# Kernel tuning notes

Measured on AMD Instinct MI355X. Metric: run time of the kernel, lower is better.

Reference implementation:

```python
import jax, jax.numpy as jnp
import numpy as np

N = 200000
E = 6400000
IN_F = 128
HID = 128
OUT_F = 16
LAYERS = 3
EPS = 1e-5


def setup_inputs() -> dict:
    key = jax.random.key(0)
    ks = jax.random.split(key, 12)
    nodes = jax.random.normal(ks[0], (N, IN_F), dtype=jnp.float32)
    src = jax.random.randint(ks[1], (E,), 0, N, dtype=jnp.int32)
    dst = jax.random.randint(ks[2], (E,), 0, N, dtype=jnp.int32)
    s_in = 1.0 / np.sqrt(IN_F)
    s_h = 1.0 / np.sqrt(HID)
    W_in = jax.random.uniform(ks[3], (IN_F, HID), jnp.float32, -s_in, s_in)
    b_in = jax.random.uniform(ks[4], (HID,), jnp.float32, -s_in, s_in)
    Ws = jax.random.uniform(ks[5], (LAYERS, HID, HID), jnp.float32, -s_h, s_h)
    bs = jax.random.uniform(ks[6], (LAYERS, HID), jnp.float32, -s_h, s_h)
    gammas = jnp.ones((LAYERS, HID), jnp.float32)
    betas = jnp.zeros((LAYERS, HID), jnp.float32)
    W_out = jax.random.uniform(ks[7], (HID, OUT_F), jnp.float32, -s_h, s_h)
    b_out = jax.random.uniform(ks[8], (OUT_F,), jnp.float32, -s_h, s_h)
    return {"nodes": nodes, "src": src, "dst": dst, "W_in": W_in, "b_in": b_in,
            "Ws": Ws, "bs": bs, "gammas": gammas, "betas": betas,
            "W_out": W_out, "b_out": b_out}


def _layernorm(x, g, b):
    mu = jnp.mean(x, axis=-1, keepdims=True)
    var = jnp.var(x, axis=-1, keepdims=True)
    return (x - mu) * jax.lax.rsqrt(var + EPS) * g + b


def reference(nodes, src, dst, W_in, b_in, Ws, bs, gammas, betas, W_out, b_out):
    # in-degree for 'gcn' aggregator normalization: (sum_neigh + self) / (deg + 1)
    deg = jax.ops.segment_sum(jnp.ones((E,), jnp.float32), dst, num_segments=N)
    inv = 1.0 / (deg + 1.0)  # [N]
    x = nodes @ W_in + b_in  # [N, HID]
    for l in range(LAYERS):
        agg = jax.ops.segment_sum(x[src], dst, num_segments=N)  # gather+scatter-add
        h = (agg + x) * inv[:, None]          # gcn mean incl. self
        h = h @ Ws[l] + bs[l]                 # fc_neigh
        h = jax.nn.relu(h)                    # activation (before norm, per DGL)
        x = _layernorm(h, gammas[l], betas[l])
    return x @ W_out + b_out  # [N, OUT_F]
```

## Files before the change

kernel.cpp:

```cpp
#include <hip/hip_runtime.h>

#define N_NODES 200000
#define N_EDGES 6400000
#define HID 128
#define OUTF 16
#define LAYERS 3
#define EPS 1e-5f

#define NRANGES 16
#define RANGE_N 12500
#define NBUCKETS 800
#define BUCKET_N 250
#define BATCH 5000
#define NBATCH (N_EDGES / BATCH)
#define RCAP 405000
#define RBLK (RCAP / BATCH)
#define BCAP 9500

#define FTILE 32

typedef unsigned int u32;

__device__ __forceinline__ unsigned short f2bf(float f){
  unsigned int u = __float_as_uint(f);
  u += 0x7fffu + ((u >> 16) & 1u);
  return (unsigned short)(u >> 16);
}
__device__ __forceinline__ u32 pack2bf(float lo, float hi){
  return (u32)f2bf(lo) | ((u32)f2bf(hi) << 16);
}


__global__ __launch_bounds__(256) void k_initcur(int* __restrict__ range_cursor,
                                                 int* __restrict__ bucket_cursor){
  int t = blockIdx.x * 256 + threadIdx.x;
  if (t < NRANGES) range_cursor[t] = t * RCAP;
  if (t < NBUCKETS) bucket_cursor[t] = t * BCAP;
}


__global__ __launch_bounds__(256) void k_p1(const int* __restrict__ src, const int* __restrict__ dst,
                                            int* __restrict__ range_cursor, u32* __restrict__ ebuf1){
  __shared__ u32 stage[BATCH];
  __shared__ int hist[NRANGES], hist2[NRANGES], hbase[NRANGES], gbase[NRANGES];
  const int tid = threadIdx.x;
  const long e0 = (long)blockIdx.x * BATCH;

  if (tid < NRANGES){ hist[tid] = 0; hist2[tid] = 0; }
  __syncthreads();
  for (int i = tid; i < BATCH; i += 256){
    int d = dst[e0 + i];
    atomicAdd(&hist[d / RANGE_N], 1);
  }
  __syncthreads();
  if (tid == 0){ int run = 0; for (int b = 0; b < NRANGES; b++){ hbase[b] = run; run += hist[b]; } }
  __syncthreads();
  if (tid < NRANGES && hist[tid] > 0) gbase[tid] = atomicAdd(&range_cursor[tid], hist[tid]);
  __syncthreads();
  for (int i = tid; i < BATCH; i += 256){
    int d = dst[e0 + i];
    int s = src[e0 + i];
    int r = d / RANGE_N;
    u32 pk = ((u32)(d - r * RANGE_N) << 18) | (u32)s;
    int p = atomicAdd(&hist2[r], 1);
    stage[hbase[r] + p] = pk;
  }
  __syncthreads();
  for (int b = 0; b < NRANGES; b++){
    int len = hist[b];
    int gb = gbase[b], hb = hbase[b];
    for (int i = tid; i < len; i += 256) ebuf1[gb + i] = stage[hb + i];
  }
}


__global__ __launch_bounds__(256) void k_p2(const u32* __restrict__ ebuf1, const int* __restrict__ range_cursor,
                                            int* __restrict__ bucket_cursor, u32* __restrict__ ebuf2){
  __shared__ u32 stage[BATCH];
  __shared__ int hist[50], hist2[50], hbase[50], gbase[50];
  const int tid = threadIdx.x;
  const int r = blockIdx.x / RBLK;
  const int chunk = blockIdx.x % RBLK;
  const int rlen = range_cursor[r] - r * RCAP;
  const int i0 = chunk * BATCH;
  const int len = min(BATCH, rlen - i0);
  if (len <= 0) return;
  const u32* seg = ebuf1 + (long)r * RCAP + i0;

  if (tid < 50){ hist[tid] = 0; hist2[tid] = 0; }
  __syncthreads();
  for (int i = tid; i < len; i += 256){
    int dl = (int)(seg[i] >> 18);
    atomicAdd(&hist[dl / BUCKET_N], 1);
  }
  __syncthreads();
  if (tid == 0){ int run = 0; for (int b = 0; b < 50; b++){ hbase[b] = run; run += hist[b]; } }
  __syncthreads();
  if (tid < 50 && hist[tid] > 0) gbase[tid] = atomicAdd(&bucket_cursor[r * 50 + tid], hist[tid]);
  __syncthreads();
  for (int i = tid; i < len; i += 256){
    u32 pk = seg[i];
    int b = (int)(pk >> 18) / BUCKET_N;
    int p = atomicAdd(&hist2[b], 1);
    stage[hbase[b] + p] = pk;
  }
  __syncthreads();
  for (int b = 0; b < 50; b++){
    int l = hist[b];
    if (l == 0) continue;
    int gb = gbase[b], hb = hbase[b];
    for (int i = tid; i < l; i += 256) ebuf2[gb + i] = stage[hb + i];
  }
}


__global__ __launch_bounds__(256) void k_scanb(const int* __restrict__ bucket_cursor,
                                               int* __restrict__ bucket_base){
  __shared__ int q[256];
  int tid = threadIdx.x;
  int v[4]; int sum4 = 0;
  if (tid < 200){
    #pragma unroll
    for (int j = 0; j < 4; j++){ int b = 4 * tid + j; v[j] = bucket_cursor[b] - b * BCAP; sum4 += v[j]; }
  }
  q[tid] = sum4; __syncthreads();
  for (int off = 1; off < 256; off <<= 1){
    int t = (tid >= off) ? q[tid - off] : 0;
    __syncthreads();
    q[tid] += t;
    __syncthreads();
  }
  if (tid < 200){
    int run = q[tid] - sum4;
    #pragma unroll
    for (int j = 0; j < 4; j++){ bucket_base[4 * tid + j] = run; run += v[j]; }
  }
}


__global__ __launch_bounds__(256) void k_p3(const u32* __restrict__ ebuf2, const int* __restrict__ bucket_cursor,
                                            const int* __restrict__ bucket_base,
                                            int* __restrict__ csr, int* __restrict__ row_start){
  __shared__ int stage[BCAP];
  __shared__ int hist[BUCKET_N], sbase[BUCKET_N], cur[BUCKET_N];
  __shared__ int q[256];
  const int tid = threadIdx.x;
  const int b = blockIdx.x;
  const int n0 = b * BUCKET_N;
  const int dl0 = (b % 50) * BUCKET_N;
  const int len = min(bucket_cursor[b] - b * BCAP, BCAP);
  const int base = bucket_base[b];
  const u32* seg = ebuf2 + (long)b * BCAP;

  if (tid < BUCKET_N){ hist[tid] = 0; cur[tid] = 0; }
  __syncthreads();
  for (int i = tid; i < len; i += 256){
    int local = (int)(seg[i] >> 18) - dl0;
    local = min(max(local, 0), BUCKET_N - 1);
    atomicAdd(&hist[local], 1);
  }
  __syncthreads();
  {
    int v = (tid < BUCKET_N) ? hist[tid] : 0;
    q[tid] = v; __syncthreads();
    for (int off = 1; off < 256; off <<= 1){
      int t = (tid >= off) ? q[tid - off] : 0;
      __syncthreads();
      q[tid] += t;
      __syncthreads();
    }
    if (tid < BUCKET_N) sbase[tid] = q[tid] - v;
  }
  __syncthreads();
  for (int i = tid; i < len; i += 256){
    u32 pk = seg[i];
    int local = (int)(pk >> 18) - dl0;
    local = min(max(local, 0), BUCKET_N - 1);
    int pos = atomicAdd(&cur[local], 1);
    stage[sbase[local] + pos] = (int)(pk & 0x3FFFFu);
  }
  __syncthreads();
  for (int i = tid; i < len; i += 256) csr[base + i] = stage[i];
  if (tid < BUCKET_N) row_start[n0 + tid] = base + sbase[tid];
  if (b == NBUCKETS - 1 && tid == 0) row_start[N_NODES] = base + len;
}


__global__ __launch_bounds__(256) void k_gemm128(const float* __restrict__ A,
    const float* __restrict__ W, const float* __restrict__ bias,
    u32* __restrict__ xbout)
{
  __shared__ float As[64][132];
  const int tid = threadIdx.x;
  const long row0 = (long)blockIdx.x * 64;

  const float4* A4 = (const float4*)(A + row0 * HID);
  for (int i = tid; i < 64 * 32; i += 256){
    int r = i >> 5, c = i & 31;
    *(float4*)&As[r][c * 4] = A4[r * 32 + c];
  }
  __syncthreads();

  const int cg = tid & 31;
  const int rg = tid >> 5;
  const int c0 = cg * 4;
  float acc[8][4];
  {
    float4 b = *(const float4*)&bias[c0];
    #pragma unroll
    for (int r = 0; r < 8; r++){ acc[r][0]=b.x; acc[r][1]=b.y; acc[r][2]=b.z; acc[r][3]=b.w; }
  }

  for (int k = 0; k < HID; k += 4){
    float4 w0 = *(const float4*)&W[(k + 0) * HID + c0];
    float4 w1 = *(const float4*)&W[(k + 1) * HID + c0];
    float4 w2 = *(const float4*)&W[(k + 2) * HID + c0];
    float4 w3 = *(const float4*)&W[(k + 3) * HID + c0];
    #pragma unroll
    for (int r = 0; r < 8; r++){
      float4 a = *(const float4*)&As[rg * 8 + r][k];
      acc[r][0] = fmaf(a.w, w3.x, fmaf(a.z, w2.x, fmaf(a.y, w1.x, fmaf(a.x, w0.x, acc[r][0]))));
      acc[r][1] = fmaf(a.w, w3.y, fmaf(a.z, w2.y, fmaf(a.y, w1.y, fmaf(a.x, w0.y, acc[r][1]))));
      acc[r][2] = fmaf(a.w, w3.z, fmaf(a.z, w2.z, fmaf(a.y, w1.z, fmaf(a.x, w0.z, acc[r][2]))));
      acc[r][3] = fmaf(a.w, w3.w, fmaf(a.z, w2.w, fmaf(a.y, w1.w, fmaf(a.x, w0.w, acc[r][3]))));
    }
  }

  #pragma unroll
  for (int r = 0; r < 8; r++){
    long row = row0 + rg * 8 + r;
    uint2 p; p.x = pack2bf(acc[r][0], acc[r][1]); p.y = pack2bf(acc[r][2], acc[r][3]);
    *(uint2*)&xbout[(row * HID + c0) >> 1] = p;
  }
}


__global__ __launch_bounds__(256) void k_fused(const int* __restrict__ row_start,
    const int* __restrict__ csr, const uint2* __restrict__ xb2,
    const float* __restrict__ W, const float* __restrict__ bias,
    const float* __restrict__ gamma, const float* __restrict__ beta,
    u32* __restrict__ xbout)
{
  __shared__ float As[FTILE][132];
  const int tid = threadIdx.x;
  const long row0 = (long)blockIdx.x * FTILE;

  {
    const int wv = tid >> 6;
    const int lane = tid & 63;
    const int half = lane >> 5, col = lane & 31;
    const uint2* xbc = xb2 + col;

    for (int i = 0; i < FTILE / 4; i++){
      const int r = wv * (FTILE / 4) + i;
      const int node = (int)row0 + r;
      const int s0 = row_start[node], s1 = row_start[node + 1];

      float4 xs = {0.f, 0.f, 0.f, 0.f};
      if (half == 0){
        uint2 sv = xb2[(long)node * 32 + col];
        xs.x = __uint_as_float(sv.x << 16);
        xs.y = __uint_as_float(sv.x & 0xffff0000u);
        xs.z = __uint_as_float(sv.y << 16);
        xs.w = __uint_as_float(sv.y & 0xffff0000u);
      }

      float a0 = 0.f, a1 = 0.f, a2 = 0.f, a3 = 0.f;
      int base = s0;
      int idx[8];
      if (base + 16 <= s1){
        #pragma unroll
        for (int j = 0; j < 8; j++) idx[j] = csr[base + 2*j + half];
      }
      while (base + 16 <= s1){
        uint2 p[8];
        #pragma unroll
        for (int j = 0; j < 8; j++) p[j] = xbc[(long)idx[j] * 32];
        base += 16;
        if (base + 16 <= s1){
          #pragma unroll
          for (int j = 0; j < 8; j++) idx[j] = csr[base + 2*j + half];
        }
        #pragma unroll
        for (int j = 0; j < 8; j++){
          a0 += __uint_as_float(p[j].x << 16);
          a1 += __uint_as_float(p[j].x & 0xffff0000u);
          a2 += __uint_as_float(p[j].y << 16);
          a3 += __uint_as_float(p[j].y & 0xffff0000u);
        }
      }
      if (base < s1){
        const int s1m1 = s1 - 1;
        int ti[8];
        #pragma unroll
        for (int j = 0; j < 8; j++) ti[j] = csr[min(base + 2*j + half, s1m1)];
        uint2 p[8];
        #pragma unroll
        for (int j = 0; j < 8; j++) p[j] = xbc[(long)ti[j] * 32];
        #pragma unroll
        for (int j = 0; j < 8; j++){
          bool act = (base + 2*j + half) < s1;
          float v0 = __uint_as_float(p[j].x << 16);
          float v1 = __uint_as_float(p[j].x & 0xffff0000u);
          float v2 = __uint_as_float(p[j].y << 16);
          float v3 = __uint_as_float(p[j].y & 0xffff0000u);
          a0 += act ? v0 : 0.f;
          a1 += act ? v1 : 0.f;
          a2 += act ? v2 : 0.f;
          a3 += act ? v3 : 0.f;
        }
      }

      a0 += __shfl_down(a0, 32);
      a1 += __shfl_down(a1, 32);
      a2 += __shfl_down(a2, 32);
      a3 += __shfl_down(a3, 32);

      if (half == 0){
        float inv = 1.f / (float)(s1 - s0 + 1);
        float4 rv;
        rv.x = (a0 + xs.x) * inv;
        rv.y = (a1 + xs.y) * inv;
        rv.z = (a2 + xs.z) * inv;
        rv.w = (a3 + xs.w) * inv;
        *(float4*)&As[r][col * 4] = rv;
      }
    }
  }
  __syncthreads();

  const int cg = tid & 31;
  const int rg = tid >> 5;
  const int c0 = cg * 4;
  float acc[4][4];
  {
    float4 b = *(const float4*)&bias[c0];
    #pragma unroll
    for (int r = 0; r < 4; r++){ acc[r][0]=b.x; acc[r][1]=b.y; acc[r][2]=b.z; acc[r][3]=b.w; }
  }

  for (int k = 0; k < HID; k += 4){
    float4 w0 = *(const float4*)&W[(k + 0) * HID + c0];
    float4 w1 = *(const float4*)&W[(k + 1) * HID + c0];
    float4 w2 = *(const float4*)&W[(k + 2) * HID + c0];
    float4 w3 = *(const float4*)&W[(k + 3) * HID + c0];
    #pragma unroll
    for (int r = 0; r < 4; r++){
      float4 a = *(const float4*)&As[rg * 4 + r][k];
      acc[r][0] = fmaf(a.w, w3.x, fmaf(a.z, w2.x, fmaf(a.y, w1.x, fmaf(a.x, w0.x, acc[r][0]))));
      acc[r][1] = fmaf(a.w, w3.y, fmaf(a.z, w2.y, fmaf(a.y, w1.y, fmaf(a.x, w0.y, acc[r][1]))));
      acc[r][2] = fmaf(a.w, w3.z, fmaf(a.z, w2.z, fmaf(a.y, w1.z, fmaf(a.x, w0.z, acc[r][2]))));
      acc[r][3] = fmaf(a.w, w3.w, fmaf(a.z, w2.w, fmaf(a.y, w1.w, fmaf(a.x, w0.w, acc[r][3]))));
    }
  }

  float s[4], s2[4];
  #pragma unroll
  for (int r = 0; r < 4; r++){
    float v0 = fmaxf(acc[r][0], 0.f);
    float v1 = fmaxf(acc[r][1], 0.f);
    float v2 = fmaxf(acc[r][2], 0.f);
    float v3 = fmaxf(acc[r][3], 0.f);
    acc[r][0] = v0; acc[r][1] = v1; acc[r][2] = v2; acc[r][3] = v3;
    s[r]  = (v0 + v1) + (v2 + v3);
    s2[r] = fmaf(v0, v0, fmaf(v1, v1, fmaf(v2, v2, v3 * v3)));
  }
  #pragma unroll
  for (int m = 1; m < 32; m <<= 1){
    #pragma unroll
    for (int r = 0; r < 4; r++){
      s[r]  += __shfl_xor(s[r],  m);
      s2[r] += __shfl_xor(s2[r], m);
    }
  }

  const float4 gm = *(const float4*)&gamma[c0];
  const float4 bt = *(const float4*)&beta[c0];
  #pragma unroll
  for (int r = 0; r < 4; r++){
    float mu = s[r] * (1.f / HID);
    float var = s2[r] * (1.f / HID) - mu * mu;
    float rs = 1.f / sqrtf(var + EPS);
    float4 v;
    v.x = (acc[r][0] - mu) * rs * gm.x + bt.x;
    v.y = (acc[r][1] - mu) * rs * gm.y + bt.y;
    v.z = (acc[r][2] - mu) * rs * gm.z + bt.z;
    v.w = (acc[r][3] - mu) * rs * gm.w + bt.w;
    long row = row0 + rg * 4 + r;
    uint2 p; p.x = pack2bf(v.x, v.y); p.y = pack2bf(v.z, v.w);
    *(uint2*)&xbout[(row * HID + c0) >> 1] = p;
  }
}


__global__ __launch_bounds__(256) void k_gemm_out(const u32* __restrict__ xb,
    const float* __restrict__ Wo, const float* __restrict__ bo, float* __restrict__ out)
{
  __shared__ float As[16][132];
  __shared__ float Wl[HID * OUTF];
  const int tid = threadIdx.x;
  const long row0 = (long)blockIdx.x * 16;
  {
    int r = tid >> 4, u = tid & 15;
    uint4 v = ((const uint4*)xb)[(row0 + r) * 16 + u];
    float* d = &As[r][u * 8];
    d[0] = __uint_as_float(v.x << 16); d[1] = __uint_as_float(v.x & 0xffff0000u);
    d[2] = __uint_as_float(v.y << 16); d[3] = __uint_as_float(v.y & 0xffff0000u);
    d[4] = __uint_as_float(v.z << 16); d[5] = __uint_as_float(v.z & 0xffff0000u);
    d[6] = __uint_as_float(v.w << 16); d[7] = __uint_as_float(v.w & 0xffff0000u);
  }
  for (int i = tid; i < HID * OUTF; i += 256) Wl[i] = Wo[i];
  __syncthreads();
  int col = tid & 15, r = tid >> 4;
  float acc = bo[col];
  for (int k = 0; k < HID; k += 4){
    float4 a = *(const float4*)&As[r][k];
    acc = fmaf(a.x, Wl[(k + 0) * OUTF + col],
          fmaf(a.y, Wl[(k + 1) * OUTF + col],
          fmaf(a.z, Wl[(k + 2) * OUTF + col],
          fmaf(a.w, Wl[(k + 3) * OUTF + col], acc))));
  }
  out[(row0 + r) * OUTF + col] = acc;
}


extern "C" void kernel_launch(void* const* d_in, const int* in_sizes, int n_in,
                              void* d_out, int out_size, void* d_ws, size_t ws_size,
                              hipStream_t stream)
{
  (void)in_sizes; (void)n_in; (void)out_size; (void)ws_size;
  const float* nodes = (const float*)d_in[0];
  const int*   src   = (const int*)d_in[1];
  const int*   dst   = (const int*)d_in[2];
  const float* W_in  = (const float*)d_in[3];
  const float* b_in  = (const float*)d_in[4];
  const float* Ws    = (const float*)d_in[5];
  const float* bs    = (const float*)d_in[6];
  const float* gam   = (const float*)d_in[7];
  const float* bet   = (const float*)d_in[8];
  const float* W_out = (const float*)d_in[9];
  const float* b_out = (const float*)d_in[10];
  float* out = (float*)d_out;

  size_t off = 0;
  auto bump = [&](size_t bytes) -> char* {
    char* p = (char*)d_ws + off;
    off = (off + bytes + 255) & ~(size_t)255;
    return p;
  };
  int* row_start     = (int*)bump((N_NODES + 1) * sizeof(int));
  int* range_cursor  = (int*)bump(NRANGES * sizeof(int));
  int* bucket_cursor = (int*)bump(NBUCKETS * sizeof(int));
  int* bucket_base   = (int*)bump((NBUCKETS + 1) * sizeof(int));
  int* csr           = (int*)bump((size_t)N_EDGES * sizeof(int));
  u32* xb0           = (u32*)bump((size_t)N_NODES * HID * sizeof(unsigned short));
  u32* xb1           = (u32*)bump((size_t)N_NODES * HID * sizeof(unsigned short));

  u32* ebuf1 = (u32*)xb0;
  u32* ebuf2 = (u32*)xb1;

  k_initcur<<<4, 256, 0, stream>>>(range_cursor, bucket_cursor);
  k_p1<<<NBATCH, 256, 0, stream>>>(src, dst, range_cursor, ebuf1);
  k_p2<<<NRANGES * RBLK, 256, 0, stream>>>(ebuf1, range_cursor, bucket_cursor, ebuf2);
  k_scanb<<<1, 256, 0, stream>>>(bucket_cursor, bucket_base);
  k_p3<<<NBUCKETS, 256, 0, stream>>>(ebuf2, bucket_cursor, bucket_base, csr, row_start);

  k_gemm128<<<N_NODES / 64, 256, 0, stream>>>(nodes, W_in, b_in, xb0);

  const u32* xbi = xb0; u32* xbo = xb1;
  for (int l = 0; l < LAYERS; l++){
    k_fused<<<N_NODES / FTILE, 256, 0, stream>>>(row_start, csr, (const uint2*)xbi,
                                                 Ws + (size_t)l * HID * HID, bs + l * HID,
                                                 gam + l * HID, bet + l * HID, xbo);
    const u32* tb = xbi; xbi = xbo; xbo = (u32*)tb;
  }

  k_gemm_out<<<N_NODES / 16, 256, 0, stream>>>(xbi, W_out, b_out, out);
}
```

Before: 1.218 ms.

## Merge input GEMM into edge partition kernel and fuse output projection into last layer

The first edge-partition pass and the input projection GEMM now run in one launch, with block ranges split between the two tasks. ebuf1 gets its own workspace buffer so the GEMM output does not collide with it. The last layer's aggregate+GEMM+LayerNorm kernel now also applies the output projection in-block, so the final bf16 activations are never written out and read back. The cost is extra workspace memory and a larger last-layer kernel that may hold more registers.

```diff
diff --git a/kernel.cpp b/kernel.cpp
--- a/kernel.cpp
+++ b/kernel.cpp
@@ -39,37 +39,90 @@
 }
 
 
-__global__ __launch_bounds__(256) void k_p1(const int* __restrict__ src, const int* __restrict__ dst,
-                                            int* __restrict__ range_cursor, u32* __restrict__ ebuf1){
-  __shared__ u32 stage[BATCH];
-  __shared__ int hist[NRANGES], hist2[NRANGES], hbase[NRANGES], gbase[NRANGES];
+__global__ __launch_bounds__(256) void k_front(const int* __restrict__ src, const int* __restrict__ dst,
+    int* __restrict__ range_cursor, u32* __restrict__ ebuf1,
+    const float* __restrict__ A, const float* __restrict__ W,
+    const float* __restrict__ bias, u32* __restrict__ xbout)
+{
+  __shared__ __align__(16) char smraw[64 * 132 * 4];
   const int tid = threadIdx.x;
-  const long e0 = (long)blockIdx.x * BATCH;
-
-  if (tid < NRANGES){ hist[tid] = 0; hist2[tid] = 0; }
-  __syncthreads();
-  for (int i = tid; i < BATCH; i += 256){
-    int d = dst[e0 + i];
-    atomicAdd(&hist[d / RANGE_N], 1);
-  }
-  __syncthreads();
-  if (tid == 0){ int run = 0; for (int b = 0; b < NRANGES; b++){ hbase[b] = run; run += hist[b]; } }
-  __syncthreads();
-  if (tid < NRANGES && hist[tid] > 0) gbase[tid] = atomicAdd(&range_cursor[tid], hist[tid]);
-  __syncthreads();
-  for (int i = tid; i < BATCH; i += 256){
-    int d = dst[e0 + i];
-    int s = src[e0 + i];
-    int r = d / RANGE_N;
-    u32 pk = ((u32)(d - r * RANGE_N) << 18) | (u32)s;
-    int p = atomicAdd(&hist2[r], 1);
-    stage[hbase[r] + p] = pk;
-  }
-  __syncthreads();
-  for (int b = 0; b < NRANGES; b++){
-    int len = hist[b];
-    int gb = gbase[b], hb = hbase[b];
-    for (int i = tid; i < len; i += 256) ebuf1[gb + i] = stage[hb + i];
+
+  if (blockIdx.x < NBATCH){
+    u32* stage = (u32*)smraw;
+    int* hist  = (int*)(smraw + 20000);
+    int* hist2 = hist + 16;
+    int* hbase = hist + 32;
+    int* gbase = hist + 48;
+    const long e0 = (long)blockIdx.x * BATCH;
+
+    if (tid < NRANGES){ hist[tid] = 0; hist2[tid] = 0; }
+    __syncthreads();
+    for (int i = tid; i < BATCH; i += 256){
+      int d = dst[e0 + i];
+      atomicAdd(&hist[d / RANGE_N], 1);
+    }
+    __syncthreads();
+    if (tid == 0){ int run = 0; for (int b = 0; b < NRANGES; b++){ hbase[b] = run; run += hist[b]; } }
+    __syncthreads();
+    if (tid < NRANGES && hist[tid] > 0) gbase[tid] = atomicAdd(&range_cursor[tid], hist[tid]);
+    __syncthreads();
+    for (int i = tid; i < BATCH; i += 256){
+      int d = dst[e0 + i];
+      int s = src[e0 + i];
+      int r = d / RANGE_N;
+      u32 pk = ((u32)(d - r * RANGE_N) << 18) | (u32)s;
+      int p = atomicAdd(&hist2[r], 1);
+      stage[hbase[r] + p] = pk;
+    }
+    __syncthreads();
+    for (int b = 0; b < NRANGES; b++){
+      int len = hist[b];
+      int gb = gbase[b], hb = hbase[b];
+      for (int i = tid; i < len; i += 256) ebuf1[gb + i] = stage[hb + i];
+    }
+    return;
+  }
+
+  float (*As)[132] = (float (*)[132])smraw;
+  const long row0 = (long)(blockIdx.x - NBATCH) * 64;
+
+  const float4* A4 = (const float4*)(A + row0 * HID);
+  for (int i = tid; i < 64 * 32; i += 256){
+    int r = i >> 5, c = i & 31;
+    *(float4*)&As[r][c * 4] = A4[r * 32 + c];
+  }
+  __syncthreads();
+
+  const int cg = tid & 31;
+  const int rg = tid >> 5;
+  const int c0 = cg * 4;
+  float acc[8][4];
+  {
+    float4 b = *(const float4*)&bias[c0];
+    #pragma unroll
+    for (int r = 0; r < 8; r++){ acc[r][0]=b.x; acc[r][1]=b.y; acc[r][2]=b.z; acc[r][3]=b.w; }
+  }
+
+  for (int k = 0; k < HID; k += 4){
+    float4 w0 = *(const float4*)&W[(k + 0) * HID + c0];
+    float4 w1 = *(const float4*)&W[(k + 1) * HID + c0];
+    float4 w2 = *(const float4*)&W[(k + 2) * HID + c0];
+    float4 w3 = *(const float4*)&W[(k + 3) * HID + c0];
+    #pragma unroll
+    for (int r = 0; r < 8; r++){
+      float4 a = *(const float4*)&As[rg * 8 + r][k];
+      acc[r][0] = fmaf(a.w, w3.x, fmaf(a.z, w2.x, fmaf(a.y, w1.x, fmaf(a.x, w0.x, acc[r][0]))));
+      acc[r][1] = fmaf(a.w, w3.y, fmaf(a.z, w2.y, fmaf(a.y, w1.y, fmaf(a.x, w0.y, acc[r][1]))));
+      acc[r][2] = fmaf(a.w, w3.z, fmaf(a.z, w2.z, fmaf(a.y, w1.z, fmaf(a.x, w0.z, acc[r][2]))));
+      acc[r][3] = fmaf(a.w, w3.w, fmaf(a.z, w2.w, fmaf(a.y, w1.w, fmaf(a.x, w0.w, acc[r][3]))));
+    }
+  }
+
+  #pragma unroll
+  for (int r = 0; r < 8; r++){
+    long row = row0 + rg * 8 + r;
+    uint2 p; p.x = pack2bf(acc[r][0], acc[r][1]); p.y = pack2bf(acc[r][2], acc[r][3]);
+    *(uint2*)&xbout[(row * HID + c0) >> 1] = p;
   }
 }
 
@@ -186,51 +239,89 @@
 }
 
 
-__global__ __launch_bounds__(256) void k_gemm128(const float* __restrict__ A,
-    const float* __restrict__ W, const float* __restrict__ bias,
-    u32* __restrict__ xbout)
+__device__ __forceinline__ void agg_tile(const int* __restrict__ row_start,
+    const int* __restrict__ csr, const uint2* __restrict__ xb2,
+    long row0, int tid, float (*As)[132])
 {
-  __shared__ float As[64][132];
-  const int tid = threadIdx.x;
-  const long row0 = (long)blockIdx.x * 64;
-
-  const float4* A4 = (const float4*)(A + row0 * HID);
-  for (int i = tid; i < 64 * 32; i += 256){
-    int r = i >> 5, c = i & 31;
-    *(float4*)&As[r][c * 4] = A4[r * 32 + c];
-  }
-  __syncthreads();
-
-  const int cg = tid & 31;
-  const int rg = tid >> 5;
-  const int c0 = cg * 4;
-  float acc[8][4];
-  {
-    float4 b = *(const float4*)&bias[c0];
-    #pragma unroll
-    for (int r = 0; r < 8; r++){ acc[r][0]=b.x; acc[r][1]=b.y; acc[r][2]=b.z; acc[r][3]=b.w; }
-  }
-
-  for (int k = 0; k < HID; k += 4){
-    float4 w0 = *(const float4*)&W[(k + 0) * HID + c0];
-    float4 w1 = *(const float4*)&W[(k + 1) * HID + c0];
-    float4 w2 = *(const float4*)&W[(k + 2) * HID + c0];
-    float4 w3 = *(const float4*)&W[(k + 3) * HID + c0];
-    #pragma unroll
-    for (int r = 0; r < 8; r++){
-      float4 a = *(const float4*)&As[rg * 8 + r][k];
-      acc[r][0] = fmaf(a.w, w3.x, fmaf(a.z, w2.x, fmaf(a.y, w1.x, fmaf(a.x, w0.x, acc[r][0]))));
-      acc[r][1] = fmaf(a.w, w3.y, fmaf(a.z, w2.y, fmaf(a.y, w1.y, fmaf(a.x, w0.y, acc[r][1]))));
-      acc[r][2] = fmaf(a.w, w3.z, fmaf(a.z, w2.z, fmaf(a.y, w1.z, fmaf(a.x, w0.z, acc[r][2]))));
-      acc[r][3] = fmaf(a.w, w3.w, fmaf(a.z, w2.w, fmaf(a.y, w1.w, fmaf(a.x, w0.w, acc[r][3]))));
-    }
-  }
-
-  #pragma unroll
-  for (int r = 0; r < 8; r++){
-    long row = row0 + rg * 8 + r;
-    uint2 p; p.x = pack2bf(acc[r][0], acc[r][1]); p.y = pack2bf(acc[r][2], acc[r][3]);
-    *(uint2*)&xbout[(row * HID + c0) >> 1] = p;
+  const int wv = tid >> 6;
+  const int lane = tid & 63;
+  const int half = lane >> 5, col = lane & 31;
+  const uint2* xbc = xb2 + col;
+
+  for (int i = 0; i < FTILE / 4; i++){
+    const int r = wv * (FTILE / 4) + i;
+    const int node = (int)row0 + r;
+    const int s0 = row_start[node], s1 = row_start[node + 1];
+
+    float4 xs = {0.f, 0.f, 0.f, 0.f};
+    if (half == 0){
+      uint2 sv = xb2[(long)node * 32 + col];
+      xs.x = __uint_as_float(sv.x << 16);
+      xs.y = __uint_as_float(sv.x & 0xffff0000u);
+      xs.z = __uint_as_float(sv.y << 16);
+      xs.w = __uint_as_float(sv.y & 0xffff0000u);
+    }
+
+    float a0 = 0.f, a1 = 0.f, a2 = 0.f, a3 = 0.f;
+    int base = s0;
+    int idx[8];
+    if (base + 16 <= s1){
+      #pragma unroll
+      for (int j = 0; j < 8; j++) idx[j] = csr[base + 2*j + half];
+    }
+    while (base + 16 <= s1){
+      uint2 p[8];
+      #pragma unroll
+      for (int j = 0; j < 8; j++) p[j] = xbc[(long)idx[j] * 32];
+      base += 16;
+      if (base + 16 <= s1){
+        #pragma unroll
+        for (int j = 0; j < 8; j++) idx[j] = csr[base + 2*j + half];
+      }
+      #pragma unroll
+      for (int j = 0; j < 8; j++){
+        a0 += __uint_as_float(p[j].x << 16);
+        a1 += __uint_as_float(p[j].x & 0xffff0000u);
+        a2 += __uint_as_float(p[j].y << 16);
+        a3 += __uint_as_float(p[j].y & 0xffff0000u);
+      }
+    }
+    if (base < s1){
+      const int s1m1 = s1 - 1;
+      int ti[8];
+      #pragma unroll
+      for (int j = 0; j < 8; j++) ti[j] = csr[min(base + 2*j + half, s1m1)];
+      uint2 p[8];
+      #pragma unroll
+      for (int j = 0; j < 8; j++) p[j] = xbc[(long)ti[j] * 32];
+      #pragma unroll
+      for (int j = 0; j < 8; j++){
+        bool act = (base + 2*j + half) < s1;
+        float v0 = __uint_as_float(p[j].x << 16);
+        float v1 = __uint_as_float(p[j].x & 0xffff0000u);
+        float v2 = __uint_as_float(p[j].y << 16);
+        float v3 = __uint_as_float(p[j].y & 0xffff0000u);
+        a0 += act ? v0 : 0.f;
+        a1 += act ? v1 : 0.f;
+        a2 += act ? v2 : 0.f;
+        a3 += act ? v3 : 0.f;
+      }
+    }
+
+    a0 += __shfl_down(a0, 32);
+    a1 += __shfl_down(a1, 32);
+    a2 += __shfl_down(a2, 32);
+    a3 += __shfl_down(a3, 32);
+
+    if (half == 0){
+      float inv = 1.f / (float)(s1 - s0 + 1);
+      float4 rv;
+      rv.x = (a0 + xs.x) * inv;
+      rv.y = (a1 + xs.y) * inv;
+      rv.z = (a2 + xs.z) * inv;
+      rv.w = (a3 + xs.w) * inv;
+      *(float4*)&As[r][col * 4] = rv;
+    }
   }
 }
 
@@ -245,88 +336,7 @@
   const int tid = threadIdx.x;
   const long row0 = (long)blockIdx.x * FTILE;
 
-  {
-    const int wv = tid >> 6;
-    const int lane = tid & 63;
-    const int half = lane >> 5, col = lane & 31;
-    const uint2* xbc = xb2 + col;
-
-    for (int i = 0; i < FTILE / 4; i++){
-      const int r = wv * (FTILE / 4) + i;
-      const int node = (int)row0 + r;
-      const int s0 = row_start[node], s1 = row_start[node + 1];
-
-      float4 xs = {0.f, 0.f, 0.f, 0.f};
-      if (half == 0){
-        uint2 sv = xb2[(long)node * 32 + col];
-        xs.x = __uint_as_float(sv.x << 16);
-        xs.y = __uint_as_float(sv.x & 0xffff0000u);
-        xs.z = __uint_as_float(sv.y << 16);
-        xs.w = __uint_as_float(sv.y & 0xffff0000u);
-      }
-
-      float a0 = 0.f, a1 = 0.f, a2 = 0.f, a3 = 0.f;
-      int base = s0;
-      int idx[8];
-      if (base + 16 <= s1){
-        #pragma unroll
-        for (int j = 0; j < 8; j++) idx[j] = csr[base + 2*j + half];
-      }
-      while (base + 16 <= s1){
-        uint2 p[8];
-        #pragma unroll
-        for (int j = 0; j < 8; j++) p[j] = xbc[(long)idx[j] * 32];
-        base += 16;
-        if (base + 16 <= s1){
-          #pragma unroll
-          for (int j = 0; j < 8; j++) idx[j] = csr[base + 2*j + half];
-        }
-        #pragma unroll
-        for (int j = 0; j < 8; j++){
-          a0 += __uint_as_float(p[j].x << 16);
-          a1 += __uint_as_float(p[j].x & 0xffff0000u);
-          a2 += __uint_as_float(p[j].y << 16);
-          a3 += __uint_as_float(p[j].y & 0xffff0000u);
-        }
-      }
-      if (base < s1){
-        const int s1m1 = s1 - 1;
-        int ti[8];
-        #pragma unroll
-        for (int j = 0; j < 8; j++) ti[j] = csr[min(base + 2*j + half, s1m1)];
-        uint2 p[8];
-        #pragma unroll
-        for (int j = 0; j < 8; j++) p[j] = xbc[(long)ti[j] * 32];
-        #pragma unroll
-        for (int j = 0; j < 8; j++){
-          bool act = (base + 2*j + half) < s1;
-          float v0 = __uint_as_float(p[j].x << 16);
-          float v1 = __uint_as_float(p[j].x & 0xffff0000u);
-          float v2 = __uint_as_float(p[j].y << 16);
-          float v3 = __uint_as_float(p[j].y & 0xffff0000u);
-          a0 += act ? v0 : 0.f;
-          a1 += act ? v1 : 0.f;
-          a2 += act ? v2 : 0.f;
-          a3 += act ? v3 : 0.f;
-        }
-      }
-
-      a0 += __shfl_down(a0, 32);
-      a1 += __shfl_down(a1, 32);
-      a2 += __shfl_down(a2, 32);
-      a3 += __shfl_down(a3, 32);
-
-      if (half == 0){
-        float inv = 1.f / (float)(s1 - s0 + 1);
-        float4 rv;
-        rv.x = (a0 + xs.x) * inv;
-        rv.y = (a1 + xs.y) * inv;
-        rv.z = (a2 + xs.z) * inv;
-        rv.w = (a3 + xs.w) * inv;
-        *(float4*)&As[r][col * 4] = rv;
-      }
-    }
-  }
+  agg_tile(row_start, csr, xb2, row0, tid, As);
   __syncthreads();
 
   const int cg = tid & 31;
@@ -393,34 +403,102 @@
 }
 
 
-__global__ __launch_bounds__(256) void k_gemm_out(const u32* __restrict__ xb,
-    const float* __restrict__ Wo, const float* __restrict__ bo, float* __restrict__ out)
+__global__ __launch_bounds__(256) void k_fused_out(const int* __restrict__ row_start,
+    const int* __restrict__ csr, const uint2* __restrict__ xb2,
+    const float* __restrict__ W, const float* __restrict__ bias,
+    const float* __restrict__ gamma, const float* __restrict__ beta,
+    const float* __restrict__ Wo, const float* __restrict__ bo,
+    float* __restrict__ out)
 {
-  __shared__ float As[16][132];
-  __shared__ float Wl[HID * OUTF];
+  __shared__ float As[FTILE][132];
   const int tid = threadIdx.x;
-  const long row0 = (long)blockIdx.x * 16;
+  const long row0 = (long)blockIdx.x * FTILE;
+
+  agg_tile(row_start, csr, xb2, row0, tid, As);
+  __syncthreads();
+
+  const int cg = tid & 31;
+  const int rg = tid >> 5;
+  const int c0 = cg * 4;
+  float acc[4][4];
   {
-    int r = tid >> 4, u = tid & 15;
-    uint4 v = ((const uint4*)xb)[(row0 + r) * 16 + u];
-    float* d = &As[r][u * 8];
-    d[0] = __uint_as_float(v.x << 16); d[1] = __uint_as_float(v.x & 0xffff0000u);
-    d[2] = __uint_as_float(v.y << 16); d[3] = __uint_as_float(v.y & 0xffff0000u);
-    d[4] = __uint_as_float(v.z << 16); d[5] = __uint_as_float(v.z & 0xffff0000u);
-    d[6] = __uint_as_float(v.w << 16); d[7] = __uint_as_float(v.w & 0xffff0000u);
-  }
-  for (int i = tid; i < HID * OUTF; i += 256) Wl[i] = Wo[i];
-  __syncthreads();
-  int col = tid & 15, r = tid >> 4;
-  float acc = bo[col];
+    float4 b = *(const float4*)&bias[c0];
+    #pragma unroll
+    for (int r = 0; r < 4; r++){ acc[r][0]=b.x; acc[r][1]=b.y; acc[r][2]=b.z; acc[r][3]=b.w; }
+  }
+
   for (int k = 0; k < HID; k += 4){
-    float4 a = *(const float4*)&As[r][k];
-    acc = fmaf(a.x, Wl[(k + 0) * OUTF + col],
-          fmaf(a.y, Wl[(k + 1) * OUTF + col],
-          fmaf(a.z, Wl[(k + 2) * OUTF + col],
-          fmaf(a.w, Wl[(k + 3) * OUTF + col], acc))));
-  }
-  out[(row0 + r) * OUTF + col] = acc;
+    float4 w0 = *(const float4*)&W[(k + 0) * HID + c0];
+    float4 w1 = *(const float4*)&W[(k + 1) * HID + c0];
+    float4 w2 = *(const float4*)&W[(k + 2) * HID + c0];
+    float4 w3 = *(const float4*)&W[(k + 3) * HID + c0];
+    #pragma unroll
+    for (int r = 0; r < 4; r++){
+      float4 a = *(const float4*)&As[rg * 4 + r][k];
+      acc[r][0] = fmaf(a.w, w3.x, fmaf(a.z, w2.x, fmaf(a.y, w1.x, fmaf(a.x, w0.x, acc[r][0]))));
+      acc[r][1] = fmaf(a.w, w3.y, fmaf(a.z, w2.y, fmaf(a.y, w1.y, fmaf(a.x, w0.y, acc[r][1]))));
+      acc[r][2] = fmaf(a.w, w3.z, fmaf(a.z, w2.z, fmaf(a.y, w1.z, fmaf(a.x, w0.z, acc[r][2]))));
+      acc[r][3] = fmaf(a.w, w3.w, fmaf(a.z, w2.w, fmaf(a.y, w1.w, fmaf(a.x, w0.w, acc[r][3]))));
+    }
+  }
+
+  float s[4], s2[4];
+  #pragma unroll
+  for (int r = 0; r < 4; r++){
+    float v0 = fmaxf(acc[r][0], 0.f);
+    float v1 = fmaxf(acc[r][1], 0.f);
+    float v2 = fmaxf(acc[r][2], 0.f);
+    float v3 = fmaxf(acc[r][3], 0.f);
+    acc[r][0] = v0; acc[r][1] = v1; acc[r][2] = v2; acc[r][3] = v3;
+    s[r]  = (v0 + v1) + (v2 + v3);
+    s2[r] = fmaf(v0, v0, fmaf(v1, v1, fmaf(v2, v2, v3 * v3)));
+  }
+  #pragma unroll
+  for (int m = 1; m < 32; m <<= 1){
+    #pragma unroll
+    for (int r = 0; r < 4; r++){
+      s[r]  += __shfl_xor(s[r],  m);
+      s2[r] += __shfl_xor(s2[r], m);
+    }
+  }
+
+  const float4 gm = *(const float4*)&gamma[c0];
+  const float4 bt = *(const float4*)&beta[c0];
+  __syncthreads();
+  #pragma unroll
+  for (int r = 0; r < 4; r++){
+    float mu = s[r] * (1.f / HID);
+    float var = s2[r] * (1.f / HID) - mu * mu;
+    float rs = 1.f / sqrtf(var + EPS);
+    float4 v;
+    v.x = (acc[r][0] - mu) * rs * gm.x + bt.x;
+    v.y = (acc[r][1] - mu) * rs * gm.y + bt.y;
+    v.z = (acc[r][2] - mu) * rs * gm.z + bt.z;
+    v.w = (acc[r][3] - mu) * rs * gm.w + bt.w;
+    u32 plo = pack2bf(v.x, v.y), phi = pack2bf(v.z, v.w);
+    float4 vb;
+    vb.x = __uint_as_float(plo << 16); vb.y = __uint_as_float(plo & 0xffff0000u);
+    vb.z = __uint_as_float(phi << 16); vb.w = __uint_as_float(phi & 0xffff0000u);
+    *(float4*)&As[rg * 4 + r][c0] = vb;
+  }
+  __syncthreads();
+
+  {
+    int col = tid & 15, rr = tid >> 4;
+    #pragma unroll
+    for (int rep = 0; rep < 2; rep++){
+      int r = rr + rep * 16;
+      float acco = bo[col];
+      for (int k = 0; k < HID; k += 4){
+        float4 a = *(const float4*)&As[r][k];
+        acco = fmaf(a.x, Wo[(k + 0) * OUTF + col],
+               fmaf(a.y, Wo[(k + 1) * OUTF + col],
+               fmaf(a.z, Wo[(k + 2) * OUTF + col],
+               fmaf(a.w, Wo[(k + 3) * OUTF + col], acco))));
+      }
+      out[(row0 + r) * OUTF + col] = acco;
+    }
+  }
 }
 
 
@@ -455,25 +533,28 @@
   int* csr           = (int*)bump((size_t)N_EDGES * sizeof(int));
   u32* xb0           = (u32*)bump((size_t)N_NODES * HID * sizeof(unsigned short));
   u32* xb1           = (u32*)bump((size_t)N_NODES * HID * sizeof(unsigned short));
-
-  u32* ebuf1 = (u32*)xb0;
+  u32* ebuf1         = (u32*)bump((size_t)NRANGES * RCAP * sizeof(u32));
+
   u32* ebuf2 = (u32*)xb1;
 
   k_initcur<<<4, 256, 0, stream>>>(range_cursor, bucket_cursor);
-  k_p1<<<NBATCH, 256, 0, stream>>>(src, dst, range_cursor, ebuf1);
+  k_front<<<NBATCH + N_NODES / 64, 256, 0, stream>>>(src, dst, range_cursor, ebuf1,
+                                                     nodes, W_in, b_in, xb0);
   k_p2<<<NRANGES * RBLK, 256, 0, stream>>>(ebuf1, range_cursor, bucket_cursor, ebuf2);
   k_scanb<<<1, 256, 0, stream>>>(bucket_cursor, bucket_base);
   k_p3<<<NBUCKETS, 256, 0, stream>>>(ebuf2, bucket_cursor, bucket_base, csr, row_start);
 
-  k_gemm128<<<N_NODES / 64, 256, 0, stream>>>(nodes, W_in, b_in, xb0);
-
   const u32* xbi = xb0; u32* xbo = xb1;
-  for (int l = 0; l < LAYERS; l++){
+  for (int l = 0; l < LAYERS - 1; l++){
     k_fused<<<N_NODES / FTILE, 256, 0, stream>>>(row_start, csr, (const uint2*)xbi,
                                                  Ws + (size_t)l * HID * HID, bs + l * HID,
                                                  gam + l * HID, bet + l * HID, xbo);
     const u32* tb = xbi; xbi = xbo; xbo = (u32*)tb;
   }
-
-  k_gemm_out<<<N_NODES / 16, 256, 0, stream>>>(xbi, W_out, b_out, out);
-}
+  k_fused_out<<<N_NODES / FTILE, 256, 0, stream>>>(row_start, csr, (const uint2*)xbi,
+                                                   Ws + (size_t)(LAYERS - 1) * HID * HID,
+                                                   bs + (LAYERS - 1) * HID,
+                                                   gam + (LAYERS - 1) * HID,
+                                                   bet + (LAYERS - 1) * HID,
+                                                   W_out, b_out, out);
+}
```

Result: slower. 1.248 ms (+2.4%).

## Merge edge partition pass with input GEMM and fold bucket scan into p3

Applied to the files above, without the earlier changes.

The first edge-partitioning pass and the input projection GEMM now run in one launch, with the block index choosing the role, so the edge bucketing and the dense GEMM can overlap on the GPU. To allow this, ebuf1 gets its own workspace buffer instead of aliasing xb0. The separate single-block bucket scan kernel is removed, and each p3 block computes its own prefix base by reducing the earlier bucket counts. The aggregation body is moved into a device helper with no behaviour change. Together this removes two launches and their serialization, at the cost of redundant prefix work in p3 (up to 800 reads per block) and extra workspace memory.

```diff
diff --git a/kernel.cpp b/kernel.cpp
--- a/kernel.cpp
+++ b/kernel.cpp
@@ -39,37 +39,90 @@
 }
 
 
-__global__ __launch_bounds__(256) void k_p1(const int* __restrict__ src, const int* __restrict__ dst,
-                                            int* __restrict__ range_cursor, u32* __restrict__ ebuf1){
-  __shared__ u32 stage[BATCH];
-  __shared__ int hist[NRANGES], hist2[NRANGES], hbase[NRANGES], gbase[NRANGES];
+__global__ __launch_bounds__(256) void k_front(const int* __restrict__ src, const int* __restrict__ dst,
+    int* __restrict__ range_cursor, u32* __restrict__ ebuf1,
+    const float* __restrict__ A, const float* __restrict__ W,
+    const float* __restrict__ bias, u32* __restrict__ xbout)
+{
+  __shared__ __align__(16) char smraw[64 * 132 * 4];
   const int tid = threadIdx.x;
-  const long e0 = (long)blockIdx.x * BATCH;
-
-  if (tid < NRANGES){ hist[tid] = 0; hist2[tid] = 0; }
-  __syncthreads();
-  for (int i = tid; i < BATCH; i += 256){
-    int d = dst[e0 + i];
-    atomicAdd(&hist[d / RANGE_N], 1);
-  }
-  __syncthreads();
-  if (tid == 0){ int run = 0; for (int b = 0; b < NRANGES; b++){ hbase[b] = run; run += hist[b]; } }
-  __syncthreads();
-  if (tid < NRANGES && hist[tid] > 0) gbase[tid] = atomicAdd(&range_cursor[tid], hist[tid]);
-  __syncthreads();
-  for (int i = tid; i < BATCH; i += 256){
-    int d = dst[e0 + i];
-    int s = src[e0 + i];
-    int r = d / RANGE_N;
-    u32 pk = ((u32)(d - r * RANGE_N) << 18) | (u32)s;
-    int p = atomicAdd(&hist2[r], 1);
-    stage[hbase[r] + p] = pk;
-  }
-  __syncthreads();
-  for (int b = 0; b < NRANGES; b++){
-    int len = hist[b];
-    int gb = gbase[b], hb = hbase[b];
-    for (int i = tid; i < len; i += 256) ebuf1[gb + i] = stage[hb + i];
+
+  if (blockIdx.x < NBATCH){
+    u32* stage = (u32*)smraw;
+    int* hist  = (int*)(smraw + 20000);
+    int* hist2 = hist + 16;
+    int* hbase = hist + 32;
+    int* gbase = hist + 48;
+    const long e0 = (long)blockIdx.x * BATCH;
+
+    if (tid < NRANGES){ hist[tid] = 0; hist2[tid] = 0; }
+    __syncthreads();
+    for (int i = tid; i < BATCH; i += 256){
+      int d = dst[e0 + i];
+      atomicAdd(&hist[d / RANGE_N], 1);
+    }
+    __syncthreads();
+    if (tid == 0){ int run = 0; for (int b = 0; b < NRANGES; b++){ hbase[b] = run; run += hist[b]; } }
+    __syncthreads();
+    if (tid < NRANGES && hist[tid] > 0) gbase[tid] = atomicAdd(&range_cursor[tid], hist[tid]);
+    __syncthreads();
+    for (int i = tid; i < BATCH; i += 256){
+      int d = dst[e0 + i];
+      int s = src[e0 + i];
+      int r = d / RANGE_N;
+      u32 pk = ((u32)(d - r * RANGE_N) << 18) | (u32)s;
+      int p = atomicAdd(&hist2[r], 1);
+      stage[hbase[r] + p] = pk;
+    }
+    __syncthreads();
+    for (int b = 0; b < NRANGES; b++){
+      int len = hist[b];
+      int gb = gbase[b], hb = hbase[b];
+      for (int i = tid; i < len; i += 256) ebuf1[gb + i] = stage[hb + i];
+    }
+    return;
+  }
+
+  float (*As)[132] = (float (*)[132])smraw;
+  const long row0 = (long)(blockIdx.x - NBATCH) * 64;
+
+  const float4* A4 = (const float4*)(A + row0 * HID);
+  for (int i = tid; i < 64 * 32; i += 256){
+    int r = i >> 5, c = i & 31;
+    *(float4*)&As[r][c * 4] = A4[r * 32 + c];
+  }
+  __syncthreads();
+
+  const int cg = tid & 31;
+  const int rg = tid >> 5;
+  const int c0 = cg * 4;
+  float acc[8][4];
+  {
+    float4 b = *(const float4*)&bias[c0];
+    #pragma unroll
+    for (int r = 0; r < 8; r++){ acc[r][0]=b.x; acc[r][1]=b.y; acc[r][2]=b.z; acc[r][3]=b.w; }
+  }
+
+  for (int k = 0; k < HID; k += 4){
+    float4 w0 = *(const float4*)&W[(k + 0) * HID + c0];
+    float4 w1 = *(const float4*)&W[(k + 1) * HID + c0];
+    float4 w2 = *(const float4*)&W[(k + 2) * HID + c0];
+    float4 w3 = *(const float4*)&W[(k + 3) * HID + c0];
+    #pragma unroll
+    for (int r = 0; r < 8; r++){
+      float4 a = *(const float4*)&As[rg * 8 + r][k];
+      acc[r][0] = fmaf(a.w, w3.x, fmaf(a.z, w2.x, fmaf(a.y, w1.x, fmaf(a.x, w0.x, acc[r][0]))));
+      acc[r][1] = fmaf(a.w, w3.y, fmaf(a.z, w2.y, fmaf(a.y, w1.y, fmaf(a.x, w0.y, acc[r][1]))));
+      acc[r][2] = fmaf(a.w, w3.z, fmaf(a.z, w2.z, fmaf(a.y, w1.z, fmaf(a.x, w0.z, acc[r][2]))));
+      acc[r][3] = fmaf(a.w, w3.w, fmaf(a.z, w2.w, fmaf(a.y, w1.w, fmaf(a.x, w0.w, acc[r][3]))));
+    }
+  }
+
+  #pragma unroll
+  for (int r = 0; r < 8; r++){
+    long row = row0 + rg * 8 + r;
+    uint2 p; p.x = pack2bf(acc[r][0], acc[r][1]); p.y = pack2bf(acc[r][2], acc[r][3]);
+    *(uint2*)&xbout[(row * HID + c0) >> 1] = p;
   }
 }
 
@@ -114,46 +167,33 @@
 }
 
 
-__global__ __launch_bounds__(256) void k_scanb(const int* __restrict__ bucket_cursor,
-                                               int* __restrict__ bucket_base){
-  __shared__ int q[256];
-  int tid = threadIdx.x;
-  int v[4]; int sum4 = 0;
-  if (tid < 200){
-    #pragma unroll
-    for (int j = 0; j < 4; j++){ int b = 4 * tid + j; v[j] = bucket_cursor[b] - b * BCAP; sum4 += v[j]; }
-  }
-  q[tid] = sum4; __syncthreads();
-  for (int off = 1; off < 256; off <<= 1){
-    int t = (tid >= off) ? q[tid - off] : 0;
-    __syncthreads();
-    q[tid] += t;
-    __syncthreads();
-  }
-  if (tid < 200){
-    int run = q[tid] - sum4;
-    #pragma unroll
-    for (int j = 0; j < 4; j++){ bucket_base[4 * tid + j] = run; run += v[j]; }
-  }
-}
-
-
 __global__ __launch_bounds__(256) void k_p3(const u32* __restrict__ ebuf2, const int* __restrict__ bucket_cursor,
-                                            const int* __restrict__ bucket_base,
                                             int* __restrict__ csr, int* __restrict__ row_start){
   __shared__ int stage[BCAP];
   __shared__ int hist[BUCKET_N], sbase[BUCKET_N], cur[BUCKET_N];
   __shared__ int q[256];
+  __shared__ int base_s;
   const int tid = threadIdx.x;
   const int b = blockIdx.x;
   const int n0 = b * BUCKET_N;
   const int dl0 = (b % 50) * BUCKET_N;
   const int len = min(bucket_cursor[b] - b * BCAP, BCAP);
-  const int base = bucket_base[b];
   const u32* seg = ebuf2 + (long)b * BCAP;
 
+  {
+    int partial = 0;
+    for (int i = tid; i < b; i += 256) partial += bucket_cursor[i] - i * BCAP;
+    q[tid] = partial; __syncthreads();
+    for (int off = 128; off > 0; off >>= 1){
+      if (tid < off) q[tid] += q[tid + off];
+      __syncthreads();
+    }
+    if (tid == 0) base_s = q[0];
+  }
+
   if (tid < BUCKET_N){ hist[tid] = 0; cur[tid] = 0; }
   __syncthreads();
+  const int base = base_s;
   for (int i = tid; i < len; i += 256){
     int local = (int)(seg[i] >> 18) - dl0;
     local = min(max(local, 0), BUCKET_N - 1);
@@ -186,51 +226,89 @@
 }
 
 
-__global__ __launch_bounds__(256) void k_gemm128(const float* __restrict__ A,
-    const float* __restrict__ W, const float* __restrict__ bias,
-    u32* __restrict__ xbout)
+__device__ __forceinline__ void agg_tile(const int* __restrict__ row_start,
+    const int* __restrict__ csr, const uint2* __restrict__ xb2,
+    long row0, int tid, float (*As)[132])
 {
-  __shared__ float As[64][132];
-  const int tid = threadIdx.x;
-  const long row0 = (long)blockIdx.x * 64;
-
-  const float4* A4 = (const float4*)(A + row0 * HID);
-  for (int i = tid; i < 64 * 32; i += 256){
-    int r = i >> 5, c = i & 31;
-    *(float4*)&As[r][c * 4] = A4[r * 32 + c];
-  }
-  __syncthreads();
-
-  const int cg = tid & 31;
-  const int rg = tid >> 5;
-  const int c0 = cg * 4;
-  float acc[8][4];
-  {
-    float4 b = *(const float4*)&bias[c0];
-    #pragma unroll
-    for (int r = 0; r < 8; r++){ acc[r][0]=b.x; acc[r][1]=b.y; acc[r][2]=b.z; acc[r][3]=b.w; }
-  }
-
-  for (int k = 0; k < HID; k += 4){
-    float4 w0 = *(const float4*)&W[(k + 0) * HID + c0];
-    float4 w1 = *(const float4*)&W[(k + 1) * HID + c0];
-    float4 w2 = *(const float4*)&W[(k + 2) * HID + c0];
-    float4 w3 = *(const float4*)&W[(k + 3) * HID + c0];
-    #pragma unroll
-    for (int r = 0; r < 8; r++){
-      float4 a = *(const float4*)&As[rg * 8 + r][k];
-      acc[r][0] = fmaf(a.w, w3.x, fmaf(a.z, w2.x, fmaf(a.y, w1.x, fmaf(a.x, w0.x, acc[r][0]))));
-      acc[r][1] = fmaf(a.w, w3.y, fmaf(a.z, w2.y, fmaf(a.y, w1.y, fmaf(a.x, w0.y, acc[r][1]))));
-      acc[r][2] = fmaf(a.w, w3.z, fmaf(a.z, w2.z, fmaf(a.y, w1.z, fmaf(a.x, w0.z, acc[r][2]))));
-      acc[r][3] = fmaf(a.w, w3.w, fmaf(a.z, w2.w, fmaf(a.y, w1.w, fmaf(a.x, w0.w, acc[r][3]))));
-    }
-  }
-
-  #pragma unroll
-  for (int r = 0; r < 8; r++){
-    long row = row0 + rg * 8 + r;
-    uint2 p; p.x = pack2bf(acc[r][0], acc[r][1]); p.y = pack2bf(acc[r][2], acc[r][3]);
-    *(uint2*)&xbout[(row * HID + c0) >> 1] = p;
+  const int wv = tid >> 6;
+  const int lane = tid & 63;
+  const int half = lane >> 5, col = lane & 31;
+  const uint2* xbc = xb2 + col;
+
+  for (int i = 0; i < FTILE / 4; i++){
+    const int r = wv * (FTILE / 4) + i;
+    const int node = (int)row0 + r;
+    const int s0 = row_start[node], s1 = row_start[node + 1];
+
+    float4 xs = {0.f, 0.f, 0.f, 0.f};
+    if (half == 0){
+      uint2 sv = xb2[(long)node * 32 + col];
+      xs.x = __uint_as_float(sv.x << 16);
+      xs.y = __uint_as_float(sv.x & 0xffff0000u);
+      xs.z = __uint_as_float(sv.y << 16);
+      xs.w = __uint_as_float(sv.y & 0xffff0000u);
+    }
+
+    float a0 = 0.f, a1 = 0.f, a2 = 0.f, a3 = 0.f;
+    int base = s0;
+    int idx[8];
+    if (base + 16 <= s1){
+      #pragma unroll
+      for (int j = 0; j < 8; j++) idx[j] = csr[base + 2*j + half];
+    }
+    while (base + 16 <= s1){
+      uint2 p[8];
+      #pragma unroll
+      for (int j = 0; j < 8; j++) p[j] = xbc[(long)idx[j] * 32];
+      base += 16;
+      if (base + 16 <= s1){
+        #pragma unroll
+        for (int j = 0; j < 8; j++) idx[j] = csr[base + 2*j + half];
+      }
+      #pragma unroll
+      for (int j = 0; j < 8; j++){
+        a0 += __uint_as_float(p[j].x << 16);
+        a1 += __uint_as_float(p[j].x & 0xffff0000u);
+        a2 += __uint_as_float(p[j].y << 16);
+        a3 += __uint_as_float(p[j].y & 0xffff0000u);
+      }
+    }
+    if (base < s1){
+      const int s1m1 = s1 - 1;
+      int ti[8];
+      #pragma unroll
+      for (int j = 0; j < 8; j++) ti[j] = csr[min(base + 2*j + half, s1m1)];
+      uint2 p[8];
+      #pragma unroll
+      for (int j = 0; j < 8; j++) p[j] = xbc[(long)ti[j] * 32];
+      #pragma unroll
+      for (int j = 0; j < 8; j++){
+        bool act = (base + 2*j + half) < s1;
+        float v0 = __uint_as_float(p[j].x << 16);
+        float v1 = __uint_as_float(p[j].x & 0xffff0000u);
+        float v2 = __uint_as_float(p[j].y << 16);
+        float v3 = __uint_as_float(p[j].y & 0xffff0000u);
+        a0 += act ? v0 : 0.f;
+        a1 += act ? v1 : 0.f;
+        a2 += act ? v2 : 0.f;
+        a3 += act ? v3 : 0.f;
+      }
+    }
+
+    a0 += __shfl_down(a0, 32);
+    a1 += __shfl_down(a1, 32);
+    a2 += __shfl_down(a2, 32);
+    a3 += __shfl_down(a3, 32);
+
+    if (half == 0){
+      float inv = 1.f / (float)(s1 - s0 + 1);
+      float4 rv;
+      rv.x = (a0 + xs.x) * inv;
+      rv.y = (a1 + xs.y) * inv;
+      rv.z = (a2 + xs.z) * inv;
+      rv.w = (a3 + xs.w) * inv;
+      *(float4*)&As[r][col * 4] = rv;
+    }
   }
 }
 
@@ -245,88 +323,7 @@
   const int tid = threadIdx.x;
   const long row0 = (long)blockIdx.x * FTILE;
 
-  {
-    const int wv = tid >> 6;
-    const int lane = tid & 63;
-    const int half = lane >> 5, col = lane & 31;
-    const uint2* xbc = xb2 + col;
-
-    for (int i = 0; i < FTILE / 4; i++){
-      const int r = wv * (FTILE / 4) + i;
-      const int node = (int)row0 + r;
-      const int s0 = row_start[node], s1 = row_start[node + 1];
-
-      float4 xs = {0.f, 0.f, 0.f, 0.f};
-      if (half == 0){
-        uint2 sv = xb2[(long)node * 32 + col];
-        xs.x = __uint_as_float(sv.x << 16);
-        xs.y = __uint_as_float(sv.x & 0xffff0000u);
-        xs.z = __uint_as_float(sv.y << 16);
-        xs.w = __uint_as_float(sv.y & 0xffff0000u);
-      }
-
-      float a0 = 0.f, a1 = 0.f, a2 = 0.f, a3 = 0.f;
-      int base = s0;
-      int idx[8];
-      if (base + 16 <= s1){
-        #pragma unroll
-        for (int j = 0; j < 8; j++) idx[j] = csr[base + 2*j + half];
-      }
-      while (base + 16 <= s1){
-        uint2 p[8];
-        #pragma unroll
-        for (int j = 0; j < 8; j++) p[j] = xbc[(long)idx[j] * 32];
-        base += 16;
-        if (base + 16 <= s1){
-          #pragma unroll
-          for (int j = 0; j < 8; j++) idx[j] = csr[base + 2*j + half];
-        }
-        #pragma unroll
-        for (int j = 0; j < 8; j++){
-          a0 += __uint_as_float(p[j].x << 16);
-          a1 += __uint_as_float(p[j].x & 0xffff0000u);
-          a2 += __uint_as_float(p[j].y << 16);
-          a3 += __uint_as_float(p[j].y & 0xffff0000u);
-        }
-      }
-      if (base < s1){
-        const int s1m1 = s1 - 1;
-        int ti[8];
-        #pragma unroll
-        for (int j = 0; j < 8; j++) ti[j] = csr[min(base + 2*j + half, s1m1)];
-        uint2 p[8];
-        #pragma unroll
-        for (int j = 0; j < 8; j++) p[j] = xbc[(long)ti[j] * 32];
-        #pragma unroll
-        for (int j = 0; j < 8; j++){
-          bool act = (base + 2*j + half) < s1;
-          float v0 = __uint_as_float(p[j].x << 16);
-          float v1 = __uint_as_float(p[j].x & 0xffff0000u);
-          float v2 = __uint_as_float(p[j].y << 16);
-          float v3 = __uint_as_float(p[j].y & 0xffff0000u);
-          a0 += act ? v0 : 0.f;
-          a1 += act ? v1 : 0.f;
-          a2 += act ? v2 : 0.f;
-          a3 += act ? v3 : 0.f;
-        }
-      }
-
-      a0 += __shfl_down(a0, 32);
-      a1 += __shfl_down(a1, 32);
-      a2 += __shfl_down(a2, 32);
-      a3 += __shfl_down(a3, 32);
-
-      if (half == 0){
-        float inv = 1.f / (float)(s1 - s0 + 1);
-        float4 rv;
-        rv.x = (a0 + xs.x) * inv;
-        rv.y = (a1 + xs.y) * inv;
-        rv.z = (a2 + xs.z) * inv;
-        rv.w = (a3 + xs.w) * inv;
-        *(float4*)&As[r][col * 4] = rv;
-      }
-    }
-  }
+  agg_tile(row_start, csr, xb2, row0, tid, As);
   __syncthreads();
 
   const int cg = tid & 31;
@@ -451,21 +448,18 @@
   int* row_start     = (int*)bump((N_NODES + 1) * sizeof(int));
   int* range_cursor  = (int*)bump(NRANGES * sizeof(int));
   int* bucket_cursor = (int*)bump(NBUCKETS * sizeof(int));
-  int* bucket_base   = (int*)bump((NBUCKETS + 1) * sizeof(int));
   int* csr           = (int*)bump((size_t)N_EDGES * sizeof(int));
   u32* xb0           = (u32*)bump((size_t)N_NODES * HID * sizeof(unsigned short));
   u32* xb1           = (u32*)bump((size_t)N_NODES * HID * sizeof(unsigned short));
-
-  u32* ebuf1 = (u32*)xb0;
+  u32* ebuf1         = (u32*)bump((size_t)NRANGES * RCAP * sizeof(u32));
+
   u32* ebuf2 = (u32*)xb1;
 
   k_initcur<<<4, 256, 0, stream>>>(range_cursor, bucket_cursor);
-  k_p1<<<NBATCH, 256, 0, stream>>>(src, dst, range_cursor, ebuf1);
+  k_front<<<NBATCH + N_NODES / 64, 256, 0, stream>>>(src, dst, range_cursor, ebuf1,
+                                                     nodes, W_in, b_in, xb0);
   k_p2<<<NRANGES * RBLK, 256, 0, stream>>>(ebuf1, range_cursor, bucket_cursor, ebuf2);
-  k_scanb<<<1, 256, 0, stream>>>(bucket_cursor, bucket_base);
-  k_p3<<<NBUCKETS, 256, 0, stream>>>(ebuf2, bucket_cursor, bucket_base, csr, row_start);
-
-  k_gemm128<<<N_NODES / 64, 256, 0, stream>>>(nodes, W_in, b_in, xb0);
+  k_p3<<<NBUCKETS, 256, 0, stream>>>(ebuf2, bucket_cursor, csr, row_start);
 
   const u32* xbi = xb0; u32* xbo = xb1;
   for (int l = 0; l < LAYERS; l++){
```

Measured after the change: 1.233 ms. About the same (+1.2%).
